# Kernel optimization log

Measured on AMD Instinct MI355X. Metric: run time of the kernel, lower is better.

The kernel has to match this reference:

```python
import jax, jax.numpy as jnp
import numpy as np

N_ITERS = 21
TEMPERATURE = 0.04


def setup_inputs() -> dict:
    key = jax.random.key(0)
    input_tensor = jax.random.normal(key, (4096, 128, 128), dtype=jnp.float32)
    return {"input_tensor": input_tensor}


def reference(input_tensor) -> jnp.ndarray:
    n = input_tensor.shape[1]
    log_alpha = input_tensor.reshape((-1, n, n)) / TEMPERATURE

    def body(_, la):
        la = la - jax.nn.logsumexp(la, axis=2, keepdims=True)  # row normalize
        la = la - jax.nn.logsumexp(la, axis=1, keepdims=True)  # col normalize
        return la

    log_alpha = jax.lax.fori_loop(0, N_ITERS, body, log_alpha)
    return jnp.exp(log_alpha)
```

## Files before the change

kernel.cpp:

```cpp
#include <hip/hip_runtime.h>

typedef short bf16x8 __attribute__((ext_vector_type(8)));
typedef float f32x4 __attribute__((ext_vector_type(4)));
typedef unsigned int u32;
typedef unsigned short u16;

#define NIT 21
#define SMIN 1e-38f
#define CSH  140.0f
#define LDSCOL 136

static __device__ __forceinline__ u16 f2bf(float f) {
    u32 u = __float_as_uint(f);
    u = (u + 0x7fffu + ((u >> 16) & 1u)) >> 16;
    return (u16)u;
}
static __device__ __forceinline__ float bf2f(u16 h) {
    return __uint_as_float(((u32)h) << 16);
}

__global__ __launch_bounds__(512)
void sinkhorn_kernel(const float* __restrict__ in, float* __restrict__ out) {
    const int t  = threadIdx.x;
    const int w  = t >> 6;
    const int lg = (t >> 4) & 3;
    const int ln = t & 15;
    const int M  = w * 16 + ln;
    const size_t mat = (size_t)blockIdx.x << 14;
    const float S = 36.067376022224085f;

    __shared__ __align__(16) u16 stage[32 * LDSCOL];
    __shared__ __align__(16) u16 a_lds[128];
    __shared__ __align__(16) u16 b_lds[128];

    bf16x8 af[4];
    bf16x8 bf[4];

    {
        const float* src = in + mat + (size_t)M * 128 + lg * 8;
        float s = 0.f;
#pragma unroll
        for (int c = 0; c < 4; ++c) {
            float4 f0 = *(const float4*)(src + c * 32);
            float4 f1 = *(const float4*)(src + c * 32 + 4);
            float e0 = __builtin_amdgcn_exp2f(fmaf(f0.x, S, -CSH));
            float e1 = __builtin_amdgcn_exp2f(fmaf(f0.y, S, -CSH));
            float e2 = __builtin_amdgcn_exp2f(fmaf(f0.z, S, -CSH));
            float e3 = __builtin_amdgcn_exp2f(fmaf(f0.w, S, -CSH));
            float e4 = __builtin_amdgcn_exp2f(fmaf(f1.x, S, -CSH));
            float e5 = __builtin_amdgcn_exp2f(fmaf(f1.y, S, -CSH));
            float e6 = __builtin_amdgcn_exp2f(fmaf(f1.z, S, -CSH));
            float e7 = __builtin_amdgcn_exp2f(fmaf(f1.w, S, -CSH));
            s += ((e0 + e1) + (e2 + e3)) + ((e4 + e5) + (e6 + e7));
            bf16x8 fr;
            fr[0] = (short)f2bf(e0); fr[1] = (short)f2bf(e1);
            fr[2] = (short)f2bf(e2); fr[3] = (short)f2bf(e3);
            fr[4] = (short)f2bf(e4); fr[5] = (short)f2bf(e5);
            fr[6] = (short)f2bf(e6); fr[7] = (short)f2bf(e7);
            af[c] = fr;
        }
        s += __shfl_xor(s, 16);
        s += __shfl_xor(s, 32);
        if (lg == 0) a_lds[M] = f2bf(__builtin_amdgcn_rcpf(fmaxf(s, SMIN)));
    }

#pragma unroll
    for (int q = 0; q < 4; ++q) {
        __syncthreads();
        if ((w >> 1) == q) {
            const int lr = ((w & 1) << 4) + ln;
#pragma unroll
            for (int c = 0; c < 4; ++c)
                *(bf16x8*)&stage[lr * LDSCOL + c * 32 + lg * 8] = af[c];
        }
        __syncthreads();
        bf16x8 fr;
#pragma unroll
        for (int j = 0; j < 8; ++j)
            fr[j] = (short)stage[(lg * 8 + j) * LDSCOL + M];
        bf[q] = fr;
    }
    __syncthreads();

    const f32x4 z4 = {0.f, 0.f, 0.f, 0.f};

#pragma unroll 1
    for (int it = 0; it < NIT; ++it) {
        {
            bf16x8 a0 = *(const bf16x8*)&a_lds[lg * 8];
            bf16x8 a1 = *(const bf16x8*)&a_lds[32 + lg * 8];
            bf16x8 a2 = *(const bf16x8*)&a_lds[64 + lg * 8];
            bf16x8 a3 = *(const bf16x8*)&a_lds[96 + lg * 8];
            f32x4 acc0 = __builtin_amdgcn_mfma_f32_16x16x32_bf16(a0, bf[0], z4, 0, 0, 0);
            f32x4 acc1 = __builtin_amdgcn_mfma_f32_16x16x32_bf16(a1, bf[1], z4, 0, 0, 0);
            acc0 = __builtin_amdgcn_mfma_f32_16x16x32_bf16(a2, bf[2], acc0, 0, 0, 0);
            acc1 = __builtin_amdgcn_mfma_f32_16x16x32_bf16(a3, bf[3], acc1, 0, 0, 0);
            if (lg == 0) {
                float v = acc0[0] + acc1[0];
                b_lds[M] = f2bf(__builtin_amdgcn_rcpf(fmaxf(v, SMIN)));
            }
        }
        __syncthreads();

        if (it < NIT - 1) {
            bf16x8 b0 = *(const bf16x8*)&b_lds[lg * 8];
            bf16x8 b1 = *(const bf16x8*)&b_lds[32 + lg * 8];
            bf16x8 b2 = *(const bf16x8*)&b_lds[64 + lg * 8];
            bf16x8 b3 = *(const bf16x8*)&b_lds[96 + lg * 8];
            f32x4 r0 = __builtin_amdgcn_mfma_f32_16x16x32_bf16(af[0], b0, z4, 0, 0, 0);
            f32x4 r1 = __builtin_amdgcn_mfma_f32_16x16x32_bf16(af[1], b1, z4, 0, 0, 0);
            r0 = __builtin_amdgcn_mfma_f32_16x16x32_bf16(af[2], b2, r0, 0, 0, 0);
            r1 = __builtin_amdgcn_mfma_f32_16x16x32_bf16(af[3], b3, r1, 0, 0, 0);
            if (ln == 0) {
#pragma unroll
                for (int r = 0; r < 4; ++r) {
                    float v = r0[r] + r1[r];
                    a_lds[w * 16 + lg * 4 + r] =
                        f2bf(__builtin_amdgcn_rcpf(fmaxf(v, SMIN)));
                }
            }
            __syncthreads();
        }
    }

    {
        float* dst = out + mat + (size_t)M * 128 + lg * 8;
        const float av = bf2f(a_lds[M]);
#pragma unroll
        for (int c = 0; c < 4; ++c) {
            const bf16x8 e = af[c];
            const bf16x8 bop = *(const bf16x8*)&b_lds[c * 32 + lg * 8];
            float4 o0, o1;
            o0.x = bf2f((u16)e[0]) * av * bf2f((u16)bop[0]);
            o0.y = bf2f((u16)e[1]) * av * bf2f((u16)bop[1]);
            o0.z = bf2f((u16)e[2]) * av * bf2f((u16)bop[2]);
            o0.w = bf2f((u16)e[3]) * av * bf2f((u16)bop[3]);
            o1.x = bf2f((u16)e[4]) * av * bf2f((u16)bop[4]);
            o1.y = bf2f((u16)e[5]) * av * bf2f((u16)bop[5]);
            o1.z = bf2f((u16)e[6]) * av * bf2f((u16)bop[6]);
            o1.w = bf2f((u16)e[7]) * av * bf2f((u16)bop[7]);
            *(float4*)(dst + c * 32)     = o0;
            *(float4*)(dst + c * 32 + 4) = o1;
        }
    }
}

extern "C" void kernel_launch(void* const* d_in, const int* in_sizes, int n_in,
                              void* d_out, int out_size, void* d_ws, size_t ws_size,
                              hipStream_t stream) {
    (void)n_in; (void)d_ws; (void)ws_size; (void)out_size;
    const float* in  = (const float*)d_in[0];
    float*       out = (float*)d_out;
    const int n_mat = in_sizes[0] / (128 * 128);
    sinkhorn_kernel<<<dim3(n_mat), dim3(512), 0, stream>>>(in, out);
}
```

Measured before the change: 146.8 us.

## Process two matrices per block to amortize barriers and interleave MFMA chains

```diff
diff --git a/kernel.cpp b/kernel.cpp
--- a/kernel.cpp
+++ b/kernel.cpp
@@ -26,18 +26,19 @@
     const int lg = (t >> 4) & 3;
     const int ln = t & 15;
     const int M  = w * 16 + ln;
-    const size_t mat = (size_t)blockIdx.x << 14;
+    const size_t mat0 = (size_t)(2 * blockIdx.x) << 14;
     const float S = 36.067376022224085f;
 
     __shared__ __align__(16) u16 stage[32 * LDSCOL];
-    __shared__ __align__(16) u16 a_lds[128];
-    __shared__ __align__(16) u16 b_lds[128];
+    __shared__ __align__(16) u16 a_lds[2][128];
+    __shared__ __align__(16) u16 b_lds[2][128];
 
-    bf16x8 af[4];
-    bf16x8 bf[4];
+    bf16x8 af[2][4];
+    bf16x8 bf[2][4];
 
-    {
-        const float* src = in + mat + (size_t)M * 128 + lg * 8;
+#pragma unroll
+    for (int pm = 0; pm < 2; ++pm) {
+        const float* src = in + mat0 + ((size_t)pm << 14) + (size_t)M * 128 + lg * 8;
         float s = 0.f;
 #pragma unroll
         for (int c = 0; c < 4; ++c) {
@@ -57,28 +58,31 @@
             fr[2] = (short)f2bf(e2); fr[3] = (short)f2bf(e3);
             fr[4] = (short)f2bf(e4); fr[5] = (short)f2bf(e5);
             fr[6] = (short)f2bf(e6); fr[7] = (short)f2bf(e7);
-            af[c] = fr;
+            af[pm][c] = fr;
         }
         s += __shfl_xor(s, 16);
         s += __shfl_xor(s, 32);
-        if (lg == 0) a_lds[M] = f2bf(__builtin_amdgcn_rcpf(fmaxf(s, SMIN)));
+        if (lg == 0) a_lds[pm][M] = f2bf(__builtin_amdgcn_rcpf(fmaxf(s, SMIN)));
     }
 
 #pragma unroll
-    for (int q = 0; q < 4; ++q) {
-        __syncthreads();
-        if ((w >> 1) == q) {
-            const int lr = ((w & 1) << 4) + ln;
+    for (int pm = 0; pm < 2; ++pm) {
 #pragma unroll
-            for (int c = 0; c < 4; ++c)
-                *(bf16x8*)&stage[lr * LDSCOL + c * 32 + lg * 8] = af[c];
+        for (int q = 0; q < 4; ++q) {
+            __syncthreads();
+            if ((w >> 1) == q) {
+                const int lr = ((w & 1) << 4) + ln;
+#pragma unroll
+                for (int c = 0; c < 4; ++c)
+                    *(bf16x8*)&stage[lr * LDSCOL + c * 32 + lg * 8] = af[pm][c];
+            }
+            __syncthreads();
+            bf16x8 fr;
+#pragma unroll
+            for (int j = 0; j < 8; ++j)
+                fr[j] = (short)stage[(lg * 8 + j) * LDSCOL + M];
+            bf[pm][q] = fr;
         }
-        __syncthreads();
-        bf16x8 fr;
-#pragma unroll
-        for (int j = 0; j < 8; ++j)
-            fr[j] = (short)stage[(lg * 8 + j) * LDSCOL + M];
-        bf[q] = fr;
     }
     __syncthreads();
 
@@ -87,49 +91,67 @@
 #pragma unroll 1
     for (int it = 0; it < NIT; ++it) {
         {
-            bf16x8 a0 = *(const bf16x8*)&a_lds[lg * 8];
-            bf16x8 a1 = *(const bf16x8*)&a_lds[32 + lg * 8];
-            bf16x8 a2 = *(const bf16x8*)&a_lds[64 + lg * 8];
-            bf16x8 a3 = *(const bf16x8*)&a_lds[96 + lg * 8];
-            f32x4 acc0 = __builtin_amdgcn_mfma_f32_16x16x32_bf16(a0, bf[0], z4, 0, 0, 0);
-            f32x4 acc1 = __builtin_amdgcn_mfma_f32_16x16x32_bf16(a1, bf[1], z4, 0, 0, 0);
-            acc0 = __builtin_amdgcn_mfma_f32_16x16x32_bf16(a2, bf[2], acc0, 0, 0, 0);
-            acc1 = __builtin_amdgcn_mfma_f32_16x16x32_bf16(a3, bf[3], acc1, 0, 0, 0);
+            bf16x8 p0 = *(const bf16x8*)&a_lds[0][lg * 8];
+            bf16x8 p1 = *(const bf16x8*)&a_lds[0][32 + lg * 8];
+            bf16x8 p2 = *(const bf16x8*)&a_lds[0][64 + lg * 8];
+            bf16x8 p3 = *(const bf16x8*)&a_lds[0][96 + lg * 8];
+            bf16x8 q0 = *(const bf16x8*)&a_lds[1][lg * 8];
+            bf16x8 q1 = *(const bf16x8*)&a_lds[1][32 + lg * 8];
+            bf16x8 q2 = *(const bf16x8*)&a_lds[1][64 + lg * 8];
+            bf16x8 q3 = *(const bf16x8*)&a_lds[1][96 + lg * 8];
+            f32x4 u0 = __builtin_amdgcn_mfma_f32_16x16x32_bf16(p0, bf[0][0], z4, 0, 0, 0);
+            f32x4 u1 = __builtin_amdgcn_mfma_f32_16x16x32_bf16(p1, bf[0][1], z4, 0, 0, 0);
+            f32x4 v0 = __builtin_amdgcn_mfma_f32_16x16x32_bf16(q0, bf[1][0], z4, 0, 0, 0);
+            f32x4 v1 = __builtin_amdgcn_mfma_f32_16x16x32_bf16(q1, bf[1][1], z4, 0, 0, 0);
+            u0 = __builtin_amdgcn_mfma_f32_16x16x32_bf16(p2, bf[0][2], u0, 0, 0, 0);
+            u1 = __builtin_amdgcn_mfma_f32_16x16x32_bf16(p3, bf[0][3], u1, 0, 0, 0);
+            v0 = __builtin_amdgcn_mfma_f32_16x16x32_bf16(q2, bf[1][2], v0, 0, 0, 0);
+            v1 = __builtin_amdgcn_mfma_f32_16x16x32_bf16(q3, bf[1][3], v1, 0, 0, 0);
             if (lg == 0) {
-                float v = acc0[0] + acc1[0];
-                b_lds[M] = f2bf(__builtin_amdgcn_rcpf(fmaxf(v, SMIN)));
+                b_lds[0][M] = f2bf(__builtin_amdgcn_rcpf(fmaxf(u0[0] + u1[0], SMIN)));
+                b_lds[1][M] = f2bf(__builtin_amdgcn_rcpf(fmaxf(v0[0] + v1[0], SMIN)));
             }
         }
         __syncthreads();
 
         if (it < NIT - 1) {
-            bf16x8 b0 = *(const bf16x8*)&b_lds[lg * 8];
-            bf16x8 b1 = *(const bf16x8*)&b_lds[32 + lg * 8];
-            bf16x8 b2 = *(const bf16x8*)&b_lds[64 + lg * 8];
-            bf16x8 b3 = *(const bf16x8*)&b_lds[96 + lg * 8];
-            f32x4 r0 = __builtin_amdgcn_mfma_f32_16x16x32_bf16(af[0], b0, z4, 0, 0, 0);
-            f32x4 r1 = __builtin_amdgcn_mfma_f32_16x16x32_bf16(af[1], b1, z4, 0, 0, 0);
-            r0 = __builtin_amdgcn_mfma_f32_16x16x32_bf16(af[2], b2, r0, 0, 0, 0);
-            r1 = __builtin_amdgcn_mfma_f32_16x16x32_bf16(af[3], b3, r1, 0, 0, 0);
+            bf16x8 p0 = *(const bf16x8*)&b_lds[0][lg * 8];
+            bf16x8 p1 = *(const bf16x8*)&b_lds[0][32 + lg * 8];
+            bf16x8 p2 = *(const bf16x8*)&b_lds[0][64 + lg * 8];
+            bf16x8 p3 = *(const bf16x8*)&b_lds[0][96 + lg * 8];
+            bf16x8 q0 = *(const bf16x8*)&b_lds[1][lg * 8];
+            bf16x8 q1 = *(const bf16x8*)&b_lds[1][32 + lg * 8];
+            bf16x8 q2 = *(const bf16x8*)&b_lds[1][64 + lg * 8];
+            bf16x8 q3 = *(const bf16x8*)&b_lds[1][96 + lg * 8];
+            f32x4 u0 = __builtin_amdgcn_mfma_f32_16x16x32_bf16(af[0][0], p0, z4, 0, 0, 0);
+            f32x4 u1 = __builtin_amdgcn_mfma_f32_16x16x32_bf16(af[0][1], p1, z4, 0, 0, 0);
+            f32x4 v0 = __builtin_amdgcn_mfma_f32_16x16x32_bf16(af[1][0], q0, z4, 0, 0, 0);
+            f32x4 v1 = __builtin_amdgcn_mfma_f32_16x16x32_bf16(af[1][1], q1, z4, 0, 0, 0);
+            u0 = __builtin_amdgcn_mfma_f32_16x16x32_bf16(af[0][2], p2, u0, 0, 0, 0);
+            u1 = __builtin_amdgcn_mfma_f32_16x16x32_bf16(af[0][3], p3, u1, 0, 0, 0);
+            v0 = __builtin_amdgcn_mfma_f32_16x16x32_bf16(af[1][2], q2, v0, 0, 0, 0);
+            v1 = __builtin_amdgcn_mfma_f32_16x16x32_bf16(af[1][3], q3, v1, 0, 0, 0);
             if (ln == 0) {
 #pragma unroll
                 for (int r = 0; r < 4; ++r) {
-                    float v = r0[r] + r1[r];
-                    a_lds[w * 16 + lg * 4 + r] =
-                        f2bf(__builtin_amdgcn_rcpf(fmaxf(v, SMIN)));
+                    a_lds[0][w * 16 + lg * 4 + r] =
+                        f2bf(__builtin_amdgcn_rcpf(fmaxf(u0[r] + u1[r], SMIN)));
+                    a_lds[1][w * 16 + lg * 4 + r] =
+                        f2bf(__builtin_amdgcn_rcpf(fmaxf(v0[r] + v1[r], SMIN)));
                 }
             }
             __syncthreads();
         }
     }
 
-    {
-        float* dst = out + mat + (size_t)M * 128 + lg * 8;
-        const float av = bf2f(a_lds[M]);
+#pragma unroll
+    for (int pm = 0; pm < 2; ++pm) {
+        float* dst = out + mat0 + ((size_t)pm << 14) + (size_t)M * 128 + lg * 8;
+        const float av = bf2f(a_lds[pm][M]);
 #pragma unroll
         for (int c = 0; c < 4; ++c) {
-            const bf16x8 e = af[c];
-            const bf16x8 bop = *(const bf16x8*)&b_lds[c * 32 + lg * 8];
+            const bf16x8 e = af[pm][c];
+            const bf16x8 bop = *(const bf16x8*)&b_lds[pm][c * 32 + lg * 8];
             float4 o0, o1;
             o0.x = bf2f((u16)e[0]) * av * bf2f((u16)bop[0]);
             o0.y = bf2f((u16)e[1]) * av * bf2f((u16)bop[1]);
@@ -152,5 +174,5 @@
     const float* in  = (const float*)d_in[0];
     float*       out = (float*)d_out;
     const int n_mat = in_sizes[0] / (128 * 128);
-    sinkhorn_kernel<<<dim3(n_mat), dim3(512), 0, stream>>>(in, out);
+    sinkhorn_kernel<<<dim3(n_mat / 2), dim3(512), 0, stream>>>(in, out);
 }
```

Measured after the change: 228.0 us. 1.55x slower.
